# Kernel optimization log

Hardware: AMD Instinct MI355X
Metric: run time of the kernel (lower is better)

The kernel has to match this reference:

```python
import jax, jax.numpy as jnp
import numpy as np

N, S, D, H = 2, 2048, 1024, 16
DH = D // H  # 64


def setup_inputs() -> dict:
    key = jax.random.key(0)
    ks = jax.random.split(key, 7)
    scale = 1.0 / np.sqrt(DH)  # ~nn.Linear default init range
    return {
        "sequences": jax.random.normal(ks[0], (N, S, D), dtype=jnp.float32),
        "Wq": jax.random.uniform(ks[1], (H, DH, DH), jnp.float32, -scale, scale),
        "bq": jax.random.uniform(ks[2], (H, DH), jnp.float32, -scale, scale),
        "Wk": jax.random.uniform(ks[3], (H, DH, DH), jnp.float32, -scale, scale),
        "bk": jax.random.uniform(ks[4], (H, DH), jnp.float32, -scale, scale),
        "Wv": jax.random.uniform(ks[5], (H, DH, DH), jnp.float32, -scale, scale),
        "bv": jax.random.uniform(ks[6], (H, DH), jnp.float32, -scale, scale),
    }


def reference(sequences, Wq, bq, Wk, bk, Wv, bv):
    n, s, d = sequences.shape
    x = sequences.reshape(n, s, H, DH)  # [N,S,H,Dh]
    # per-head Linear: y = x @ W^T + b, batched over heads
    q = jnp.einsum('nshd,hed->nshe', x, Wq) + bq  # [N,S,H,Dh]
    k = jnp.einsum('nshd,hed->nshe', x, Wk) + bk
    v = jnp.einsum('nshd,hed->nshe', x, Wv) + bv
    # attention: scores [N,H,S,S]
    scores = jnp.einsum('nqhd,nkhd->nhqk', q, k) / jnp.sqrt(jnp.float32(DH))
    w = jax.nn.softmax(scores, axis=-1)
    out = jnp.einsum('nhqk,nkhd->nqhd', w, v)  # [N,S,H,Dh]
    return out.reshape(n, s, d)
```

## Files before the change

### kernel.cpp

```cpp
#include <hip/hip_runtime.h>
#include <hip/hip_bf16.h>


#define NB 2
#define SS 2048
#define DM 1024
#define NH 16
#define DHd 64

typedef __attribute__((ext_vector_type(8))) short bf16x8;
typedef __attribute__((ext_vector_type(4))) float f32x4;

union U8 { bf16x8 v; unsigned short u[8]; };

__device__ __forceinline__ unsigned short f2b(float x) {
    __hip_bfloat16 h = __float2bfloat16(x);
    return *reinterpret_cast<unsigned short*>(&h);
}

__device__ __forceinline__ bf16x8 pack8(float4 a, float4 b) {
    U8 t;
    t.u[0] = f2b(a.x); t.u[1] = f2b(a.y); t.u[2] = f2b(a.z); t.u[3] = f2b(a.w);
    t.u[4] = f2b(b.x); t.u[5] = f2b(b.y); t.u[6] = f2b(b.z); t.u[7] = f2b(b.w);
    return t.v;
}

__device__ __forceinline__ int swz(int row, int ch) {
    return row * 64 + ((ch ^ (row & 7)) * 8);
}

__global__ __launch_bounds__(256) void qkv_proj(
    const float* __restrict__ seq,
    const float* __restrict__ Wq, const float* __restrict__ bq,
    const float* __restrict__ Wk, const float* __restrict__ bk,
    const float* __restrict__ Wv, const float* __restrict__ bv,
    unsigned short* __restrict__ Q, unsigned short* __restrict__ K,
    unsigned short* __restrict__ Vt)
{
    __shared__ unsigned short Xl[128 * 64];
    __shared__ unsigned short Wl[3 * 64 * 64];

    const int tid = threadIdx.x;
    const int wv = tid >> 6, L = tid & 63, lo = L & 15, qd = L >> 4;
    const int bi = blockIdx.x;
    const int nh = bi >> 4, sb = bi & 15;
    const int h = nh & (NH - 1), n = nh >> 4;
    const int s0 = sb * 128;

#pragma unroll
    for (int i = 0; i < 4; ++i) {
        int idx = tid + i * 256;
        int r = idx >> 3, ch = idx & 7;
        const float* src = seq + ((size_t)(n * SS + s0 + r)) * DM + h * DHd + ch * 8;
        float4 a = ((const float4*)src)[0];
        float4 b = ((const float4*)src)[1];
        *(bf16x8*)&Xl[swz(r, ch)] = pack8(a, b);
    }
#pragma unroll
    for (int i = 0; i < 6; ++i) {
        int idx = tid + i * 256;
        int mat = idx >> 9;
        int rem = idx & 511;
        int e = rem >> 3, ch = rem & 7;
        const float* Wm = (mat == 0) ? Wq : (mat == 1) ? Wk : Wv;
        const float* src = Wm + (size_t)(h * DHd + e) * DHd + ch * 8;
        float4 a = ((const float4*)src)[0];
        float4 b = ((const float4*)src)[1];
        *(bf16x8*)&Wl[mat * 4096 + swz(e, ch)] = pack8(a, b);
    }
    __syncthreads();

    bf16x8 xf[2][2];
#pragma unroll
    for (int st = 0; st < 2; ++st)
#pragma unroll
        for (int kt = 0; kt < 2; ++kt)
            xf[st][kt] = *(const bf16x8*)&Xl[swz(wv * 32 + st * 16 + lo, kt * 4 + qd)];

#pragma unroll
    for (int m2 = 0; m2 < 2; ++m2) {
        const unsigned short* Wb = &Wl[m2 * 4096];
        const float* bias = m2 ? bk : bq;
        unsigned short* O = m2 ? K : Q;
        const float sc = m2 ? 1.0f : 0.125f;

        f32x4 acc[4][2];
#pragma unroll
        for (int et = 0; et < 4; ++et) {
            float4 bb = *(const float4*)&bias[h * DHd + et * 16 + qd * 4];
#pragma unroll
            for (int st = 0; st < 2; ++st)
                acc[et][st] = (f32x4){bb.x, bb.y, bb.z, bb.w};
        }
#pragma unroll
        for (int et = 0; et < 4; ++et) {
            bf16x8 wf0 = *(const bf16x8*)&Wb[swz(et * 16 + lo, qd)];
            bf16x8 wf1 = *(const bf16x8*)&Wb[swz(et * 16 + lo, 4 + qd)];
#pragma unroll
            for (int st = 0; st < 2; ++st) {
                acc[et][st] = __builtin_amdgcn_mfma_f32_16x16x32_bf16(
                    wf0, xf[st][0], acc[et][st], 0, 0, 0);
                acc[et][st] = __builtin_amdgcn_mfma_f32_16x16x32_bf16(
                    wf1, xf[st][1], acc[et][st], 0, 0, 0);
            }
        }
#pragma unroll
        for (int et = 0; et < 4; ++et)
#pragma unroll
            for (int st = 0; st < 2; ++st) {
                int s = s0 + wv * 32 + st * 16 + lo;
                ushort4 w;
                w.x = f2b(acc[et][st][0] * sc); w.y = f2b(acc[et][st][1] * sc);
                w.z = f2b(acc[et][st][2] * sc); w.w = f2b(acc[et][st][3] * sc);
                *(ushort4*)&O[((size_t)nh * SS + s) * DHd + et * 16 + qd * 4] = w;
            }
    }

    {
        const unsigned short* Wb = &Wl[2 * 4096];
        float bvv[4];
#pragma unroll
        for (int et = 0; et < 4; ++et) bvv[et] = bv[h * DHd + et * 16 + lo];

        f32x4 acc[2][4];
#pragma unroll
        for (int st = 0; st < 2; ++st)
#pragma unroll
            for (int et = 0; et < 4; ++et)
                acc[st][et] = (f32x4){bvv[et], bvv[et], bvv[et], bvv[et]};
#pragma unroll
        for (int et = 0; et < 4; ++et) {
            bf16x8 wf0 = *(const bf16x8*)&Wb[swz(et * 16 + lo, qd)];
            bf16x8 wf1 = *(const bf16x8*)&Wb[swz(et * 16 + lo, 4 + qd)];
#pragma unroll
            for (int st = 0; st < 2; ++st) {
                acc[st][et] = __builtin_amdgcn_mfma_f32_16x16x32_bf16(
                    xf[st][0], wf0, acc[st][et], 0, 0, 0);
                acc[st][et] = __builtin_amdgcn_mfma_f32_16x16x32_bf16(
                    xf[st][1], wf1, acc[st][et], 0, 0, 0);
            }
        }
#pragma unroll
        for (int st = 0; st < 2; ++st)
#pragma unroll
            for (int et = 0; et < 4; ++et) {
                int e = et * 16 + lo;
                int s = s0 + wv * 32 + st * 16 + qd * 4;
                ushort4 w;
                w.x = f2b(acc[st][et][0]); w.y = f2b(acc[st][et][1]);
                w.z = f2b(acc[st][et][2]); w.w = f2b(acc[st][et][3]);
                *(ushort4*)&Vt[((size_t)nh * DHd + e) * SS + s] = w;
            }
    }
}

#define PSTR 72

__global__ __launch_bounds__(256) void attn(
    const unsigned short* __restrict__ Qg, const unsigned short* __restrict__ Kg,
    const unsigned short* __restrict__ Vg, float* __restrict__ out)
{
    __shared__ unsigned short Kl[64 * 64];
    __shared__ unsigned short Vl[64 * 64];
    __shared__ unsigned short Pl[4][32 * PSTR];

    const int tid = threadIdx.x;
    const int wv = tid >> 6, L = tid & 63, lo = L & 15, qd = L >> 4;
    const int bi = blockIdx.x;
    const int nh = bi >> 4, qblk = bi & 15;
    const int h = nh & (NH - 1), n = nh >> 4;
    const int q0 = qblk * 128 + wv * 32;

    const unsigned short* Qnh = Qg + (size_t)nh * SS * DHd;
    const unsigned short* Knh = Kg + (size_t)nh * SS * DHd;
    const unsigned short* Vnh = Vg + (size_t)nh * DHd * SS;

    bf16x8 qf[2][2];
#pragma unroll
    for (int ct = 0; ct < 2; ++ct)
#pragma unroll
        for (int kt = 0; kt < 2; ++kt)
            qf[ct][kt] = *(const bf16x8*)(Qnh + (size_t)(q0 + ct * 16 + lo) * DHd
                                          + kt * 32 + qd * 8);

    f32x4 oacc[4][2];
#pragma unroll
    for (int rt = 0; rt < 4; ++rt)
#pragma unroll
        for (int ct = 0; ct < 2; ++ct)
            oacc[rt][ct] = (f32x4){0.f, 0.f, 0.f, 0.f};

    float m[2] = {-1e30f, -1e30f}, l[2] = {0.f, 0.f};

    for (int kv0 = 0; kv0 < SS; kv0 += 64) {
        __syncthreads();
#pragma unroll
        for (int i = 0; i < 2; ++i) {
            int idx = tid + i * 256;
            int r = idx >> 3, ch = idx & 7;
            *(uint4*)&Kl[swz(r, ch)] =
                *(const uint4*)(Knh + (size_t)(kv0 + r) * DHd + ch * 8);
            *(uint4*)&Vl[swz(r, ch)] =
                *(const uint4*)(Vnh + (size_t)r * SS + kv0 + ch * 8);
        }
        __syncthreads();

        f32x4 sacc[4][2];
#pragma unroll
        for (int rt = 0; rt < 4; ++rt)
#pragma unroll
            for (int ct = 0; ct < 2; ++ct)
                sacc[rt][ct] = (f32x4){0.f, 0.f, 0.f, 0.f};
#pragma unroll
        for (int rt = 0; rt < 4; ++rt)
#pragma unroll
            for (int kt = 0; kt < 2; ++kt) {
                bf16x8 kf = *(const bf16x8*)&Kl[swz(rt * 16 + lo, kt * 4 + qd)];
#pragma unroll
                for (int ct = 0; ct < 2; ++ct)
                    sacc[rt][ct] = __builtin_amdgcn_mfma_f32_16x16x32_bf16(
                        kf, qf[ct][kt], sacc[rt][ct], 0, 0, 0);
            }

#pragma unroll
        for (int ct = 0; ct < 2; ++ct) {
            float mx = sacc[0][ct][0];
#pragma unroll
            for (int rt = 0; rt < 4; ++rt)
#pragma unroll
                for (int r = 0; r < 4; ++r)
                    mx = fmaxf(mx, sacc[rt][ct][r]);
            mx = fmaxf(mx, __shfl_xor(mx, 16, 64));
            mx = fmaxf(mx, __shfl_xor(mx, 32, 64));
            const float mo = m[ct];
            const float mn = fmaxf(mo, mx);
            const float corr = __expf(mo - mn);
            float rs = 0.f;
#pragma unroll
            for (int rt = 0; rt < 4; ++rt) {
                float p0 = __expf(sacc[rt][ct][0] - mn);
                float p1 = __expf(sacc[rt][ct][1] - mn);
                float p2 = __expf(sacc[rt][ct][2] - mn);
                float p3 = __expf(sacc[rt][ct][3] - mn);
                rs += (p0 + p1) + (p2 + p3);
                ushort4 w;
                w.x = f2b(p0); w.y = f2b(p1); w.z = f2b(p2); w.w = f2b(p3);
                *(ushort4*)&Pl[wv][(ct * 16 + lo) * PSTR + rt * 16 + qd * 4] = w;
            }
            rs += __shfl_xor(rs, 16, 64);
            rs += __shfl_xor(rs, 32, 64);
            l[ct] = l[ct] * corr + rs;
            m[ct] = mn;
#pragma unroll
            for (int rt = 0; rt < 4; ++rt)
#pragma unroll
                for (int r = 0; r < 4; ++r)
                    oacc[rt][ct][r] *= corr;
        }

#pragma unroll
        for (int kt = 0; kt < 2; ++kt) {
            bf16x8 pf[2];
#pragma unroll
            for (int ct = 0; ct < 2; ++ct)
                pf[ct] = *(const bf16x8*)&Pl[wv][(ct * 16 + lo) * PSTR
                                                 + kt * 32 + qd * 8];
#pragma unroll
            for (int rt = 0; rt < 4; ++rt) {
                bf16x8 vf = *(const bf16x8*)&Vl[swz(rt * 16 + lo, kt * 4 + qd)];
#pragma unroll
                for (int ct = 0; ct < 2; ++ct)
                    oacc[rt][ct] = __builtin_amdgcn_mfma_f32_16x16x32_bf16(
                        vf, pf[ct], oacc[rt][ct], 0, 0, 0);
            }
        }
    }

#pragma unroll
    for (int ct = 0; ct < 2; ++ct) {
        const float inv = 1.0f / l[ct];
        const int s = q0 + ct * 16 + lo;
#pragma unroll
        for (int rt = 0; rt < 4; ++rt) {
            float4 o;
            o.x = oacc[rt][ct][0] * inv; o.y = oacc[rt][ct][1] * inv;
            o.z = oacc[rt][ct][2] * inv; o.w = oacc[rt][ct][3] * inv;
            *(float4*)&out[((size_t)n * SS + s) * DM + h * DHd
                           + rt * 16 + qd * 4] = o;
        }
    }
}

extern "C" void kernel_launch(void* const* d_in, const int* in_sizes, int n_in,
                              void* d_out, int out_size, void* d_ws, size_t ws_size,
                              hipStream_t stream) {
    const float* seq = (const float*)d_in[0];
    const float* Wq  = (const float*)d_in[1];
    const float* bq  = (const float*)d_in[2];
    const float* Wk  = (const float*)d_in[3];
    const float* bk  = (const float*)d_in[4];
    const float* Wv  = (const float*)d_in[5];
    const float* bv  = (const float*)d_in[6];
    float* out = (float*)d_out;

    const size_t per = (size_t)NB * NH * SS * DHd;
    unsigned short* Q  = (unsigned short*)d_ws;
    unsigned short* K  = Q + per;
    unsigned short* Vt = K + per;

    qkv_proj<<<512, 256, 0, stream>>>(seq, Wq, bq, Wk, bk, Wv, bv, Q, K, Vt);
    attn<<<512, 256, 0, stream>>>(Q, K, Vt, out);
}
```

Measured before the change: 158.0 us.

## Prefetch K/V tiles in registers, use exp2 with lazy rescale, and raise MFMA priority

The attention loop now loads the next K/V tile into registers while the current tile is being computed, which overlaps global latency with MFMA work. Softmax switches to exp2 by folding log2(e) into the Q scale. The running max is updated and the accumulator rescaled only when a new max exceeds the old one by a threshold, and the row-sum reduction across lanes is deferred to the end. s_setprio raises wave priority around the MFMA sections. The lazy rescale lets exp2 values grow up to 2^3 before rescaling, so it relies on staying within fp32 and bf16 range.

```diff
diff --git a/kernel.cpp b/kernel.cpp
--- a/kernel.cpp
+++ b/kernel.cpp
@@ -28,6 +28,8 @@
 __device__ __forceinline__ int swz(int row, int ch) {
     return row * 64 + ((ch ^ (row & 7)) * 8);
 }
+
+#define QSCALE 0.18033688011112042f
 
 __global__ __launch_bounds__(256) void qkv_proj(
     const float* __restrict__ seq,
@@ -82,7 +84,7 @@
         const unsigned short* Wb = &Wl[m2 * 4096];
         const float* bias = m2 ? bk : bq;
         unsigned short* O = m2 ? K : Q;
-        const float sc = m2 ? 1.0f : 0.125f;
+        const float sc = m2 ? 1.0f : QSCALE;
 
         f32x4 acc[4][2];
 #pragma unroll
@@ -155,6 +157,7 @@
 }
 
 #define PSTR 72
+#define THR 3.0f
 
 __global__ __launch_bounds__(256) void attn(
     const unsigned short* __restrict__ Qg, const unsigned short* __restrict__ Kg,
@@ -175,6 +178,8 @@
     const unsigned short* Knh = Kg + (size_t)nh * SS * DHd;
     const unsigned short* Vnh = Vg + (size_t)nh * DHd * SS;
 
+    const int r0 = tid >> 3, c0 = tid & 7;
+
     bf16x8 qf[2][2];
 #pragma unroll
     for (int ct = 0; ct < 2; ++ct)
@@ -190,20 +195,29 @@
         for (int ct = 0; ct < 2; ++ct)
             oacc[rt][ct] = (f32x4){0.f, 0.f, 0.f, 0.f};
 
-    float m[2] = {-1e30f, -1e30f}, l[2] = {0.f, 0.f};
-
-    for (int kv0 = 0; kv0 < SS; kv0 += 64) {
+    float m[2] = {-1e30f, -1e30f};
+    float l[2] = {0.f, 0.f};
+
+    uint4 ks0 = *(const uint4*)(Knh + (size_t)r0 * DHd + c0 * 8);
+    uint4 ks1 = *(const uint4*)(Knh + (size_t)(r0 + 32) * DHd + c0 * 8);
+    uint4 vs0 = *(const uint4*)(Vnh + (size_t)r0 * SS + c0 * 8);
+    uint4 vs1 = *(const uint4*)(Vnh + (size_t)(r0 + 32) * SS + c0 * 8);
+
+    for (int t = 0; t < SS / 64; ++t) {
         __syncthreads();
-#pragma unroll
-        for (int i = 0; i < 2; ++i) {
-            int idx = tid + i * 256;
-            int r = idx >> 3, ch = idx & 7;
-            *(uint4*)&Kl[swz(r, ch)] =
-                *(const uint4*)(Knh + (size_t)(kv0 + r) * DHd + ch * 8);
-            *(uint4*)&Vl[swz(r, ch)] =
-                *(const uint4*)(Vnh + (size_t)r * SS + kv0 + ch * 8);
-        }
+        *(uint4*)&Kl[swz(r0, c0)]      = ks0;
+        *(uint4*)&Kl[swz(r0 + 32, c0)] = ks1;
+        *(uint4*)&Vl[swz(r0, c0)]      = vs0;
+        *(uint4*)&Vl[swz(r0 + 32, c0)] = vs1;
         __syncthreads();
+
+        if (t + 1 < SS / 64) {
+            const int kn = (t + 1) * 64;
+            ks0 = *(const uint4*)(Knh + (size_t)(kn + r0) * DHd + c0 * 8);
+            ks1 = *(const uint4*)(Knh + (size_t)(kn + r0 + 32) * DHd + c0 * 8);
+            vs0 = *(const uint4*)(Vnh + (size_t)r0 * SS + kn + c0 * 8);
+            vs1 = *(const uint4*)(Vnh + (size_t)(r0 + 32) * SS + kn + c0 * 8);
+        }
 
         f32x4 sacc[4][2];
 #pragma unroll
@@ -211,6 +225,7 @@
 #pragma unroll
             for (int ct = 0; ct < 2; ++ct)
                 sacc[rt][ct] = (f32x4){0.f, 0.f, 0.f, 0.f};
+        __builtin_amdgcn_s_setprio(1);
 #pragma unroll
         for (int rt = 0; rt < 4; ++rt)
 #pragma unroll
@@ -221,6 +236,7 @@
                     sacc[rt][ct] = __builtin_amdgcn_mfma_f32_16x16x32_bf16(
                         kf, qf[ct][kt], sacc[rt][ct], 0, 0, 0);
             }
+        __builtin_amdgcn_s_setprio(0);
 
 #pragma unroll
         for (int ct = 0; ct < 2; ++ct) {
@@ -232,32 +248,34 @@
                     mx = fmaxf(mx, sacc[rt][ct][r]);
             mx = fmaxf(mx, __shfl_xor(mx, 16, 64));
             mx = fmaxf(mx, __shfl_xor(mx, 32, 64));
-            const float mo = m[ct];
-            const float mn = fmaxf(mo, mx);
-            const float corr = __expf(mo - mn);
+            if (__any(mx > m[ct] + THR)) {
+                const float mn = fmaxf(m[ct], mx);
+                const float corr = __builtin_amdgcn_exp2f(m[ct] - mn);
+                l[ct] *= corr;
+#pragma unroll
+                for (int rt = 0; rt < 4; ++rt)
+#pragma unroll
+                    for (int r = 0; r < 4; ++r)
+                        oacc[rt][ct][r] *= corr;
+                m[ct] = mn;
+            }
+            const float mb = m[ct];
             float rs = 0.f;
 #pragma unroll
             for (int rt = 0; rt < 4; ++rt) {
-                float p0 = __expf(sacc[rt][ct][0] - mn);
-                float p1 = __expf(sacc[rt][ct][1] - mn);
-                float p2 = __expf(sacc[rt][ct][2] - mn);
-                float p3 = __expf(sacc[rt][ct][3] - mn);
+                float p0 = __builtin_amdgcn_exp2f(sacc[rt][ct][0] - mb);
+                float p1 = __builtin_amdgcn_exp2f(sacc[rt][ct][1] - mb);
+                float p2 = __builtin_amdgcn_exp2f(sacc[rt][ct][2] - mb);
+                float p3 = __builtin_amdgcn_exp2f(sacc[rt][ct][3] - mb);
                 rs += (p0 + p1) + (p2 + p3);
                 ushort4 w;
                 w.x = f2b(p0); w.y = f2b(p1); w.z = f2b(p2); w.w = f2b(p3);
                 *(ushort4*)&Pl[wv][(ct * 16 + lo) * PSTR + rt * 16 + qd * 4] = w;
             }
-            rs += __shfl_xor(rs, 16, 64);
-            rs += __shfl_xor(rs, 32, 64);
-            l[ct] = l[ct] * corr + rs;
-            m[ct] = mn;
-#pragma unroll
-            for (int rt = 0; rt < 4; ++rt)
-#pragma unroll
-                for (int r = 0; r < 4; ++r)
-                    oacc[rt][ct][r] *= corr;
-        }
-
+            l[ct] += rs;
+        }
+
+        __builtin_amdgcn_s_setprio(1);
 #pragma unroll
         for (int kt = 0; kt < 2; ++kt) {
             bf16x8 pf[2];
@@ -274,11 +292,15 @@
                         vf, pf[ct], oacc[rt][ct], 0, 0, 0);
             }
         }
+        __builtin_amdgcn_s_setprio(0);
     }
 
 #pragma unroll
     for (int ct = 0; ct < 2; ++ct) {
-        const float inv = 1.0f / l[ct];
+        float lt = l[ct];
+        lt += __shfl_xor(lt, 16, 64);
+        lt += __shfl_xor(lt, 32, 64);
+        const float inv = 1.0f / lt;
         const int s = q0 + ct * 16 + lo;
 #pragma unroll
         for (int rt = 0; rt < 4; ++rt) {
```

Result: faster. 144.9 us (-8.3%).
